# Kernel optimization log

Measured on AMD Instinct MI355X. Metric: run time of the kernel, lower is better.

## Reference

```python
import jax, jax.numpy as jnp
import numpy as np

B, T, I, O = 64, 1024, 512, 512
EPS = 1e-5


def setup_inputs() -> dict:
    key = jax.random.key(0)
    k1, k2 = jax.random.split(key)
    x = jax.random.normal(k1, (B, T, I), dtype=jnp.float32)
    W = jax.random.normal(k2, (4 * O, I + O), dtype=jnp.float32) * 0.02
    gamma = jnp.ones((4, O), dtype=jnp.float32)
    beta = jnp.zeros((4, O), dtype=jnp.float32)
    init_hx = jnp.zeros((1, O), dtype=jnp.float32)
    init_cx = jnp.zeros((1, O), dtype=jnp.float32)
    return {"x": x, "W": W, "gamma": gamma, "beta": beta,
            "init_hx": init_hx, "init_cx": init_cx}


def reference(x, W, gamma, beta, init_hx, init_cx):
    b = x.shape[0]
    o = init_hx.shape[-1]

    def step(carry, xt):
        h, c = carry
        # fused gate projection: [B, I+O] @ [I+O, 4O] -> [B, 4, O]
        z = jnp.concatenate([xt, h], axis=-1) @ W.T
        z = z.reshape(b, 4, o)
        # LayerNorm over the last TWO dims (gate axis + feature axis), per torch nn.LayerNorm([4, O])
        mu = jnp.mean(z, axis=(-2, -1), keepdims=True)
        var = jnp.var(z, axis=(-2, -1), keepdims=True)
        zn = (z - mu) * jax.lax.rsqrt(var + EPS) * gamma + beta
        gates = jax.nn.sigmoid(zn[:, :3])  # f, i, o gates
        f_g, i_g, o_g = gates[:, 0], gates[:, 1], gates[:, 2]
        h_state = jax.nn.gelu(zn[:, 3], approximate=False)  # dropout = identity (eval)
        c_new = f_g * c + i_g * h_state
        h_new = o_g * c_new
        return (h_new, c_new), h_new

    h0 = jnp.broadcast_to(init_hx, (b, o))
    c0 = jnp.broadcast_to(init_cx, (b, o))
    x_t = jnp.swapaxes(x, 0, 1)  # [T, B, I]
    _, hs = jax.lax.scan(step, (h0, c0), x_t)
    return jnp.swapaxes(hs, 0, 1)  # [B, T, O]
```

## Files before the change

### kernel.cpp

```cpp
#include <hip/hip_runtime.h>
#include <math.h>

#define B_  64
#define T_  1024
#define I_  512
#define O_  512
#define NZ  2048
#define KW  1024
#define EPS 1e-5f

#define SREC 32
#define OSL  16

typedef short bf8_t  __attribute__((ext_vector_type(8)));
typedef float f32x4  __attribute__((ext_vector_type(4)));

__device__ __forceinline__ unsigned short f2bf(float f) {
  union { float f; unsigned u; } v; v.f = f;
  unsigned r = v.u + 0x7FFFu + ((v.u >> 16) & 1u);
  return (unsigned short)(r >> 16);
}
__device__ __forceinline__ float bf2f(unsigned short b) {
  union { unsigned u; float f; } v; v.u = ((unsigned)b) << 16;
  return v.f;
}

__global__ __launch_bounds__(256) void init_all(
    const float* __restrict__ init_hx,
    unsigned short* __restrict__ h, unsigned* __restrict__ sync) {
  int idx = blockIdx.x * 256 + threadIdx.x;
  if (idx < 2048) sync[idx] = 0u;
  if (idx < B_ * O_) h[idx] = f2bf(init_hx[idx & (O_ - 1)]);
}

__global__ __launch_bounds__(256) void zx_gemm(
    const float* __restrict__ x, const float* __restrict__ W,
    unsigned short* __restrict__ zx) {
  const int tid  = threadIdx.x;
  const int w    = tid >> 6;
  const int lane = tid & 63;
  const int q    = lane >> 4;
  const int col  = lane & 15;
  const int mblk = blockIdx.x >> 5;
  const int nblk = blockIdx.x & 31;
  const int m0   = mblk * 64 + w * 16;
  const int n0   = nblk * 64;

  f32x4 acc[4];
  #pragma unroll
  for (int i = 0; i < 4; ++i) acc[i] = (f32x4){0.f, 0.f, 0.f, 0.f};

  const float* __restrict__ arow = x + (size_t)(m0 + col) * I_;

  for (int ks = 0; ks < 16; ++ks) {
    const int k0 = ks * 32 + q * 8;
    float4 a0 = *(const float4*)(arow + k0);
    float4 a1 = *(const float4*)(arow + k0 + 4);
    bf8_t af;
    af[0] = (short)f2bf(a0.x); af[1] = (short)f2bf(a0.y);
    af[2] = (short)f2bf(a0.z); af[3] = (short)f2bf(a0.w);
    af[4] = (short)f2bf(a1.x); af[5] = (short)f2bf(a1.y);
    af[6] = (short)f2bf(a1.z); af[7] = (short)f2bf(a1.w);
    #pragma unroll
    for (int nt = 0; nt < 4; ++nt) {
      const float* __restrict__ brow =
          W + (size_t)(n0 + nt * 16 + col) * KW + k0;
      float4 b0 = *(const float4*)(brow);
      float4 b1 = *(const float4*)(brow + 4);
      bf8_t bfr;
      bfr[0] = (short)f2bf(b0.x); bfr[1] = (short)f2bf(b0.y);
      bfr[2] = (short)f2bf(b0.z); bfr[3] = (short)f2bf(b0.w);
      bfr[4] = (short)f2bf(b1.x); bfr[5] = (short)f2bf(b1.y);
      bfr[6] = (short)f2bf(b1.z); bfr[7] = (short)f2bf(b1.w);
      acc[nt] = __builtin_amdgcn_mfma_f32_16x16x32_bf16(af, bfr, acc[nt], 0, 0, 0);
    }
  }
  #pragma unroll
  for (int nt = 0; nt < 4; ++nt)
    #pragma unroll
    for (int r = 0; r < 4; ++r) {
      int m = m0 + 4 * q + r;
      zx[(size_t)m * NZ + n0 + nt * 16 + col] = f2bf(acc[nt][r]);
    }
}

__global__ __launch_bounds__(256) void lstm_rec(
    const float* __restrict__ W, const float* __restrict__ gamma,
    const float* __restrict__ beta, const float* __restrict__ init_cx,
    const unsigned short* __restrict__ zx, unsigned short* __restrict__ h,
    unsigned long long* __restrict__ part8, float* __restrict__ out,
    unsigned* __restrict__ flags) {

  __shared__ unsigned short whlds[64 * 520];
  __shared__ float mr[128];

  const int tid  = threadIdx.x;
  const int w    = tid >> 6;
  const int lane = tid & 63;
  const int q    = lane >> 4;
  const int col  = lane & 15;
  const int s    = blockIdx.x;
  const int o    = s * OSL + col;

  for (int e4 = tid; e4 < 64 * 128; e4 += 256) {
    int r  = e4 >> 7;
    int k4 = (e4 & 127) * 4;
    int g  = r >> 4, np = r & 15;
    const float4 v =
        *(const float4*)(W + (size_t)(512 * g + OSL * s + np) * KW + I_ + k4);
    unsigned short* d = &whlds[r * 520 + k4];
    d[0] = f2bf(v.x); d[1] = f2bf(v.y); d[2] = f2bf(v.z); d[3] = f2bf(v.w);
  }

  float gma[4], bta[4], c_reg[4];
  #pragma unroll
  for (int g = 0; g < 4; ++g) { gma[g] = gamma[g * O_ + o]; bta[g] = beta[g * O_ + o]; }
  { float c0 = init_cx[o];
    #pragma unroll
    for (int r = 0; r < 4; ++r) c_reg[r] = c0; }

  unsigned short zxl[16];
  #pragma unroll
  for (int g = 0; g < 4; ++g)
    #pragma unroll
    for (int r = 0; r < 4; ++r) {
      int b = 16 * w + 4 * q + r;
      zxl[g * 4 + r] = zx[((size_t)b * T_ + 0) * NZ + g * O_ + OSL * s + col];
    }

  __syncthreads();

  for (int t = 0; t < T_; ++t) {
    unsigned long long araw[32];
    const unsigned short* hrow = h + (16 * w + col) * O_;
    #pragma unroll
    for (int ks = 0; ks < 16; ++ks) {
      const unsigned long long* p =
          (const unsigned long long*)(hrow + ks * 32 + q * 8);
      araw[2 * ks]     = __hip_atomic_load(p,     __ATOMIC_RELAXED, __HIP_MEMORY_SCOPE_AGENT);
      araw[2 * ks + 1] = __hip_atomic_load(p + 1, __ATOMIC_RELAXED, __HIP_MEMORY_SCOPE_AGENT);
    }

    f32x4 acc[4];
    #pragma unroll
    for (int g = 0; g < 4; ++g) acc[g] = (f32x4){0.f, 0.f, 0.f, 0.f};

    #pragma unroll
    for (int ks = 0; ks < 16; ++ks) {
      union { unsigned long long u[2]; bf8_t v; } au;
      au.u[0] = araw[2 * ks]; au.u[1] = araw[2 * ks + 1];
      #pragma unroll
      for (int g = 0; g < 4; ++g) {
        bf8_t bfr = *(const bf8_t*)(&whlds[(g * 16 + col) * 520 + ks * 32 + q * 8]);
        acc[g] = __builtin_amdgcn_mfma_f32_16x16x32_bf16(au.v, bfr, acc[g], 0, 0, 0);
      }
    }

    float z[16];
    float s1[4], s2[4];
    #pragma unroll
    for (int r = 0; r < 4; ++r) { s1[r] = 0.f; s2[r] = 0.f; }
    #pragma unroll
    for (int g = 0; g < 4; ++g)
      #pragma unroll
      for (int r = 0; r < 4; ++r) {
        float zv = acc[g][r] + bf2f(zxl[g * 4 + r]);
        z[g * 4 + r] = zv;
        s1[r] += zv;
        s2[r] += zv * zv;
      }
    #pragma unroll
    for (int m = 1; m < 16; m <<= 1) {
      #pragma unroll
      for (int r = 0; r < 4; ++r) {
        s1[r] += __shfl_xor(s1[r], m, 64);
        s2[r] += __shfl_xor(s2[r], m, 64);
      }
    }
    if (col == 0) {
      #pragma unroll
      for (int r = 0; r < 4; ++r) {
        int b = 16 * w + 4 * q + r;
        union { float f[2]; unsigned long long u; } pv;
        pv.f[0] = s1[r]; pv.f[1] = s2[r];
        __hip_atomic_store(&part8[s * 64 + b], pv.u,
                           __ATOMIC_RELAXED, __HIP_MEMORY_SCOPE_AGENT);
      }
    }

    __syncthreads();
    {
      const unsigned tgt = 2u * (unsigned)t + 1u;
      if (tid == 0)
        __hip_atomic_store(&flags[s * 16], tgt,
                           __ATOMIC_RELAXED, __HIP_MEMORY_SCOPE_AGENT);
      const unsigned* fp = &flags[(tid & 31) * 16];
      while (__hip_atomic_load(fp, __ATOMIC_RELAXED, __HIP_MEMORY_SCOPE_AGENT) < tgt) {}
    }

    if (tid < 64) {
      float S1 = 0.f, S2 = 0.f;
      #pragma unroll
      for (int j = 0; j < 32; ++j) {
        union { float f[2]; unsigned long long u; } pv;
        pv.u = __hip_atomic_load(&part8[j * 64 + tid],
                                 __ATOMIC_RELAXED, __HIP_MEMORY_SCOPE_AGENT);
        S1 += pv.f[0]; S2 += pv.f[1];
      }
      float mean = S1 * (1.f / NZ);
      float var  = S2 * (1.f / NZ) - mean * mean;
      mr[2 * tid]     = mean;
      mr[2 * tid + 1] = rsqrtf(var + EPS);
    }
    __syncthreads();

    #pragma unroll
    for (int r = 0; r < 4; ++r) {
      int b = 16 * w + 4 * q + r;
      float mean = mr[2 * b], rstd = mr[2 * b + 1];
      float zn0 = (z[0 * 4 + r] - mean) * rstd * gma[0] + bta[0];
      float zn1 = (z[1 * 4 + r] - mean) * rstd * gma[1] + bta[1];
      float zn2 = (z[2 * 4 + r] - mean) * rstd * gma[2] + bta[2];
      float zn3 = (z[3 * 4 + r] - mean) * rstd * gma[3] + bta[3];
      float fg = 1.f / (1.f + expf(-zn0));
      float ig = 1.f / (1.f + expf(-zn1));
      float og = 1.f / (1.f + expf(-zn2));
      float gg = 0.5f * zn3 * (1.f + erff(zn3 * 0.70710678118654752f));
      float cn = fg * c_reg[r] + ig * gg;
      float hn = og * cn;
      c_reg[r] = cn;
      __hip_atomic_store(&h[b * O_ + o], f2bf(hn),
                         __ATOMIC_RELAXED, __HIP_MEMORY_SCOPE_AGENT);
      out[((size_t)b * T_ + t) * O_ + o] = hn;
    }

    if (t + 1 < T_) {
      __syncthreads();
      const unsigned tgt = 2u * (unsigned)t + 2u;
      if (tid == 0)
        __hip_atomic_store(&flags[s * 16], tgt,
                           __ATOMIC_RELAXED, __HIP_MEMORY_SCOPE_AGENT);
      #pragma unroll
      for (int g = 0; g < 4; ++g)
        #pragma unroll
        for (int r = 0; r < 4; ++r) {
          int b = 16 * w + 4 * q + r;
          zxl[g * 4 + r] =
              zx[((size_t)b * T_ + (t + 1)) * NZ + g * O_ + OSL * s + col];
        }
      const unsigned* fp = &flags[(tid & 31) * 16];
      while (__hip_atomic_load(fp, __ATOMIC_RELAXED, __HIP_MEMORY_SCOPE_AGENT) < tgt) {}
    }
  }
}

extern "C" void kernel_launch(void* const* d_in, const int* in_sizes, int n_in,
                              void* d_out, int out_size, void* d_ws, size_t ws_size,
                              hipStream_t stream) {
  const float* x       = (const float*)d_in[0];
  const float* W       = (const float*)d_in[1];
  const float* gamma   = (const float*)d_in[2];
  const float* beta    = (const float*)d_in[3];
  const float* init_hx = (const float*)d_in[4];
  const float* init_cx = (const float*)d_in[5];
  float* out = (float*)d_out;
  (void)in_sizes; (void)n_in; (void)out_size; (void)ws_size;

  char* ws = (char*)d_ws;
  unsigned*           flags = (unsigned*)(ws);
  unsigned long long* part8 = (unsigned long long*)(ws + 8192);
  unsigned short*     h     = (unsigned short*)(ws + 32768);
  unsigned short*     zx    = (unsigned short*)(ws + (1 << 20));

  init_all<<<128, 256, 0, stream>>>(init_hx, h, flags);
  zx_gemm<<<32768, 256, 0, stream>>>(x, W, zx);
  lstm_rec<<<SREC, 256, 0, stream>>>(W, gamma, beta, init_cx, zx, h, part8, out, flags);
}
```

Before: 10.89 ms.

## Use counter-based grid barriers, distributed stats reduction, and prepacked bf16 W

Replaces the per-block flag array barrier (every thread polling 32 flags) with two monotonically increasing atomic counters, one per barrier phase, and has each wave reduce the LayerNorm partial sums itself through shuffles instead of one wave writing them to LDS behind an extra __syncthreads. The partial-sum layout is transposed so each batch row's 32 partials are contiguous. The output store is moved after the barrier arrival so it overlaps the wait. A separate kernel pre-converts the input-projection part of W to bf16 so the zx GEMM loads bf16 fragments directly; this adds a launch and uses more workspace, and all blocks contending on a single counter may add atomic traffic.

```diff
diff --git a/kernel.cpp b/kernel.cpp
--- a/kernel.cpp
+++ b/kernel.cpp
@@ -33,8 +33,18 @@
   if (idx < B_ * O_) h[idx] = f2bf(init_hx[idx & (O_ - 1)]);
 }
 
+__global__ __launch_bounds__(256) void wx_bf16(
+    const float* __restrict__ W, unsigned short* __restrict__ Wbf) {
+  int idx = blockIdx.x * 256 + threadIdx.x;
+  int n  = idx >> 7;
+  int k4 = (idx & 127) * 4;
+  float4 v = *(const float4*)(W + (size_t)n * KW + k4);
+  unsigned short* d = Wbf + (size_t)n * 512 + k4;
+  d[0] = f2bf(v.x); d[1] = f2bf(v.y); d[2] = f2bf(v.z); d[3] = f2bf(v.w);
+}
+
 __global__ __launch_bounds__(256) void zx_gemm(
-    const float* __restrict__ x, const float* __restrict__ W,
+    const float* __restrict__ x, const unsigned short* __restrict__ Wbf,
     unsigned short* __restrict__ zx) {
   const int tid  = threadIdx.x;
   const int w    = tid >> 6;
@@ -63,15 +73,7 @@
     af[6] = (short)f2bf(a1.z); af[7] = (short)f2bf(a1.w);
     #pragma unroll
     for (int nt = 0; nt < 4; ++nt) {
-      const float* __restrict__ brow =
-          W + (size_t)(n0 + nt * 16 + col) * KW + k0;
-      float4 b0 = *(const float4*)(brow);
-      float4 b1 = *(const float4*)(brow + 4);
-      bf8_t bfr;
-      bfr[0] = (short)f2bf(b0.x); bfr[1] = (short)f2bf(b0.y);
-      bfr[2] = (short)f2bf(b0.z); bfr[3] = (short)f2bf(b0.w);
-      bfr[4] = (short)f2bf(b1.x); bfr[5] = (short)f2bf(b1.y);
-      bfr[6] = (short)f2bf(b1.z); bfr[7] = (short)f2bf(b1.w);
+      bf8_t bfr = *(const bf8_t*)(Wbf + (size_t)(n0 + nt * 16 + col) * 512 + k0);
       acc[nt] = __builtin_amdgcn_mfma_f32_16x16x32_bf16(af, bfr, acc[nt], 0, 0, 0);
     }
   }
@@ -92,7 +94,6 @@
     unsigned* __restrict__ flags) {
 
   __shared__ unsigned short whlds[64 * 520];
-  __shared__ float mr[128];
 
   const int tid  = threadIdx.x;
   const int w    = tid >> 6;
@@ -119,6 +120,9 @@
     #pragma unroll
     for (int r = 0; r < 4; ++r) c_reg[r] = c0; }
 
+  unsigned* cnt1 = flags;
+  unsigned* cnt2 = flags + 64;
+
   unsigned short zxl[16];
   #pragma unroll
   for (int g = 0; g < 4; ++g)
@@ -183,41 +187,41 @@
         int b = 16 * w + 4 * q + r;
         union { float f[2]; unsigned long long u; } pv;
         pv.f[0] = s1[r]; pv.f[1] = s2[r];
-        __hip_atomic_store(&part8[s * 64 + b], pv.u,
+        __hip_atomic_store(&part8[(size_t)b * SREC + s], pv.u,
                            __ATOMIC_RELAXED, __HIP_MEMORY_SCOPE_AGENT);
       }
     }
 
     __syncthreads();
+    if (tid == 0)
+      __hip_atomic_fetch_add(cnt1, 1u, __ATOMIC_RELAXED, __HIP_MEMORY_SCOPE_AGENT);
     {
-      const unsigned tgt = 2u * (unsigned)t + 1u;
-      if (tid == 0)
-        __hip_atomic_store(&flags[s * 16], tgt,
-                           __ATOMIC_RELAXED, __HIP_MEMORY_SCOPE_AGENT);
-      const unsigned* fp = &flags[(tid & 31) * 16];
-      while (__hip_atomic_load(fp, __ATOMIC_RELAXED, __HIP_MEMORY_SCOPE_AGENT) < tgt) {}
-    }
-
-    if (tid < 64) {
-      float S1 = 0.f, S2 = 0.f;
-      #pragma unroll
-      for (int j = 0; j < 32; ++j) {
+      const unsigned tgt = (unsigned)(t + 1) * SREC;
+      while (__hip_atomic_load(cnt1, __ATOMIC_RELAXED, __HIP_MEMORY_SCOPE_AGENT) < tgt) {}
+    }
+
+    float S1 = 0.f, S2 = 0.f;
+    {
+      const int brow = 16 * w + (lane & 15);
+      const unsigned long long* pp = &part8[(size_t)brow * SREC + (lane >> 4) * 8];
+      #pragma unroll
+      for (int i = 0; i < 8; ++i) {
         union { float f[2]; unsigned long long u; } pv;
-        pv.u = __hip_atomic_load(&part8[j * 64 + tid],
-                                 __ATOMIC_RELAXED, __HIP_MEMORY_SCOPE_AGENT);
+        pv.u = __hip_atomic_load(pp + i, __ATOMIC_RELAXED, __HIP_MEMORY_SCOPE_AGENT);
         S1 += pv.f[0]; S2 += pv.f[1];
       }
-      float mean = S1 * (1.f / NZ);
-      float var  = S2 * (1.f / NZ) - mean * mean;
-      mr[2 * tid]     = mean;
-      mr[2 * tid + 1] = rsqrtf(var + EPS);
-    }
-    __syncthreads();
-
+    }
+    S1 += __shfl_xor(S1, 16, 64); S2 += __shfl_xor(S2, 16, 64);
+    S1 += __shfl_xor(S1, 32, 64); S2 += __shfl_xor(S2, 32, 64);
+    float mean_l = S1 * (1.f / NZ);
+    float rstd_l = rsqrtf(S2 * (1.f / NZ) - mean_l * mean_l + EPS);
+
+    float hnl[4];
     #pragma unroll
     for (int r = 0; r < 4; ++r) {
       int b = 16 * w + 4 * q + r;
-      float mean = mr[2 * b], rstd = mr[2 * b + 1];
+      float mean = __shfl(mean_l, 4 * q + r, 64);
+      float rstd = __shfl(rstd_l, 4 * q + r, 64);
       float zn0 = (z[0 * 4 + r] - mean) * rstd * gma[0] + bta[0];
       float zn1 = (z[1 * 4 + r] - mean) * rstd * gma[1] + bta[1];
       float zn2 = (z[2 * 4 + r] - mean) * rstd * gma[2] + bta[2];
@@ -229,17 +233,20 @@
       float cn = fg * c_reg[r] + ig * gg;
       float hn = og * cn;
       c_reg[r] = cn;
+      hnl[r] = hn;
       __hip_atomic_store(&h[b * O_ + o], f2bf(hn),
                          __ATOMIC_RELAXED, __HIP_MEMORY_SCOPE_AGENT);
-      out[((size_t)b * T_ + t) * O_ + o] = hn;
     }
 
     if (t + 1 < T_) {
       __syncthreads();
-      const unsigned tgt = 2u * (unsigned)t + 2u;
       if (tid == 0)
-        __hip_atomic_store(&flags[s * 16], tgt,
-                           __ATOMIC_RELAXED, __HIP_MEMORY_SCOPE_AGENT);
+        __hip_atomic_fetch_add(cnt2, 1u, __ATOMIC_RELAXED, __HIP_MEMORY_SCOPE_AGENT);
+      #pragma unroll
+      for (int r = 0; r < 4; ++r) {
+        int b = 16 * w + 4 * q + r;
+        out[((size_t)b * T_ + t) * O_ + o] = hnl[r];
+      }
       #pragma unroll
       for (int g = 0; g < 4; ++g)
         #pragma unroll
@@ -248,8 +255,14 @@
           zxl[g * 4 + r] =
               zx[((size_t)b * T_ + (t + 1)) * NZ + g * O_ + OSL * s + col];
         }
-      const unsigned* fp = &flags[(tid & 31) * 16];
-      while (__hip_atomic_load(fp, __ATOMIC_RELAXED, __HIP_MEMORY_SCOPE_AGENT) < tgt) {}
+      const unsigned tgt = (unsigned)(t + 1) * SREC;
+      while (__hip_atomic_load(cnt2, __ATOMIC_RELAXED, __HIP_MEMORY_SCOPE_AGENT) < tgt) {}
+    } else {
+      #pragma unroll
+      for (int r = 0; r < 4; ++r) {
+        int b = 16 * w + 4 * q + r;
+        out[((size_t)b * T_ + t) * O_ + o] = hnl[r];
+      }
     }
   }
 }
@@ -270,9 +283,11 @@
   unsigned*           flags = (unsigned*)(ws);
   unsigned long long* part8 = (unsigned long long*)(ws + 8192);
   unsigned short*     h     = (unsigned short*)(ws + 32768);
-  unsigned short*     zx    = (unsigned short*)(ws + (1 << 20));
+  unsigned short*     Wbf   = (unsigned short*)(ws + (1 << 20));
+  unsigned short*     zx    = (unsigned short*)(ws + (4 << 20));
 
   init_all<<<128, 256, 0, stream>>>(init_hx, h, flags);
-  zx_gemm<<<32768, 256, 0, stream>>>(x, W, zx);
+  wx_bf16<<<1024, 256, 0, stream>>>(W, Wbf);
+  zx_gemm<<<32768, 256, 0, stream>>>(x, Wbf, zx);
   lstm_rec<<<SREC, 256, 0, stream>>>(W, gamma, beta, init_cx, zx, h, part8, out, flags);
 }
```

After: 11.70 ms. 1.07x slower.
